# Kernel optimization log

Hardware: AMD Instinct MI355X
Metric: run time of the kernel (lower is better)

## Reference

```python
import jax, jax.numpy as jnp
import numpy as np

BIN_SIZE = 256
TOP_K = 16


def setup_inputs() -> dict:
    key = jax.random.key(0)
    kx, kc = jax.random.split(key)
    x = jax.random.normal(kx, (2, 4096, 512), dtype=jnp.float32)
    codebook = jax.random.normal(kc, (512, 16), dtype=jnp.float32)  # (feature_dim, max_num_bins//2)
    return {"x": x, "codebook": codebook}


def reference(x, codebook):
    B, N, F = x.shape
    n_bins = N // BIN_SIZE  # 16
    # LSH bucket assignment: project onto random hyperplanes, pick argmax of [p, -p]
    mul = x @ codebook[:, : n_bins // 2]                      # (B, N, n_bins//2)
    cmul = jnp.concatenate([mul, -mul], axis=-1)              # (B, N, n_bins)
    bin_idx = jnp.argmax(cmul, axis=-1)                       # (B, N)
    # argsort-based binning: equal-size bins of points sorted by bucket id
    bins_split = jnp.argsort(bin_idx, axis=-1).reshape(B, n_bins, BIN_SIZE)
    # gather points into bins: (B, n_bins, bin_size, F)
    points_binned = jnp.take_along_axis(x[:, None, :, :], bins_split[..., None], axis=2)
    # intra-bin dense similarity + sigmoid
    dm = jax.nn.sigmoid(jnp.einsum('bnif,bnjf->bnij', points_binned, points_binned))
    vals, idx = jax.lax.top_k(dm, TOP_K)                      # (B, n_bins, bin_size, k)
    # map local bin indices back to global point indices
    dst = jnp.take_along_axis(bins_split[:, :, None, :], idx, axis=-1)  # (B, nb, bs, k)
    src = jnp.broadcast_to(bins_split[..., None], dst.shape)
    b = jnp.broadcast_to(jnp.arange(B)[:, None, None, None], dst.shape)
    # dense equivalent of the coalesced batched sparse_coo_tensor of size (N, N)
    out = jnp.zeros((B, N, N), dtype=x.dtype).at[b, src, dst].add(vals)
    return out
```

## Files before the change

### kernel.cpp

```cpp
#include <hip/hip_runtime.h>
#include <stdint.h>
#include <math.h>

#define NPTS 4096
#define NF 512
#define NBINS 16
#define BSZ 256
#define TOPK 16
#define NBATCH 2
#define KSPLIT 4
#define SPART (NBATCH * NBINS * BSZ * BSZ)

typedef float vf4 __attribute__((ext_vector_type(4)));

__global__ __launch_bounds__(256) void k_assign(const float* __restrict__ x,
                                                const float* __restrict__ cb,
                                                int* __restrict__ bin_idx) {
    int gw   = (blockIdx.x * 256 + threadIdx.x) >> 6;
    int lane = threadIdx.x & 63;
    const float* row = x + (size_t)gw * NF;
    float acc[8];
#pragma unroll
    for (int j = 0; j < 8; j++) acc[j] = 0.f;
    for (int f = lane; f < NF; f += 64) {
        float xv = row[f];
        const float4* c = (const float4*)(cb + f * 16);
        float4 c0 = c[0], c1 = c[1];
        acc[0] += xv * c0.x; acc[1] += xv * c0.y; acc[2] += xv * c0.z; acc[3] += xv * c0.w;
        acc[4] += xv * c1.x; acc[5] += xv * c1.y; acc[6] += xv * c1.z; acc[7] += xv * c1.w;
    }
#pragma unroll
    for (int off = 32; off > 0; off >>= 1) {
#pragma unroll
        for (int j = 0; j < 8; j++) acc[j] += __shfl_xor(acc[j], off, 64);
    }
    if (lane == 0) {
        float best = acc[0]; int bi = 0;
#pragma unroll
        for (int j = 1; j < 8; j++) { if (acc[j] > best) { best = acc[j]; bi = j; } }
#pragma unroll
        for (int j = 0; j < 8; j++) { float v = -acc[j]; if (v > best) { best = v; bi = 8 + j; } }
        bin_idx[gw] = bi;
    }
}

__global__ __launch_bounds__(256) void k_sort(const int* __restrict__ bin_idx,
                                              int* __restrict__ order) {
    __shared__ int hist[NBINS][256];
    __shared__ int segsum[NBINS][16];
    __shared__ int segoff[NBINS][16];
    __shared__ int totals[NBINS];
    __shared__ int keybase[NBINS];
    int b = blockIdx.x, t = threadIdx.x;
    const int* bi = bin_idx + b * NPTS;
#pragma unroll
    for (int j = 0; j < NBINS; j++) hist[j][t] = 0;
    int base = t * 16;
    for (int i = 0; i < 16; i++) { int k = bi[base + i]; hist[k][t]++; }
    __syncthreads();
    {
        int j = t >> 4, sg = t & 15, s = 0;
#pragma unroll
        for (int u = 0; u < 16; u++) s += hist[j][sg * 16 + u];
        segsum[j][sg] = s;
    }
    __syncthreads();
    if (t < NBINS) {
        int run = 0;
#pragma unroll
        for (int sg = 0; sg < 16; sg++) { int c = segsum[t][sg]; segoff[t][sg] = run; run += c; }
        totals[t] = run;
    }
    __syncthreads();
    if (t == 0) {
        int run = 0;
#pragma unroll
        for (int j = 0; j < NBINS; j++) { keybase[j] = run; run += totals[j]; }
    }
    __syncthreads();
    {
        int j = t >> 4, sg = t & 15;
        int run = segoff[j][sg];
#pragma unroll
        for (int u = 0; u < 16; u++) { int c = hist[j][sg * 16 + u]; hist[j][sg * 16 + u] = run; run += c; }
    }
    __syncthreads();
    int* ob = order + b * NPTS;
    for (int i = 0; i < 16; i++) {
        int k = bi[base + i];
        int o = hist[k][t];
        hist[k][t] = o + 1;
        ob[keybase[k] + o] = base + i;
    }
}

__global__ __launch_bounds__(256, 2) void k_gemm(const float* __restrict__ x,
                                                 const int* __restrict__ order,
                                                 float* __restrict__ S) {
    int blk = blockIdx.x;
    int kh  = blk & 3;
    int tn  = (blk >> 2) & 1;
    int tm  = (blk >> 3) & 1;
    int bin = (blk >> 4) & 15;
    int b   = blk >> 8;
    int t  = threadIdx.x;
    int tx = t & 15, ty = t >> 4;
    __shared__ int   idxA[128];
    __shared__ int   idxB[128];
    __shared__ float Asl[32][132];
    __shared__ float Bsl[32][132];
    int ob = b * NPTS + bin * BSZ;
    if (t < 128) idxA[t] = order[ob + tm * 128 + t];
    else         idxB[t - 128] = order[ob + tn * 128 + (t - 128)];
    __syncthreads();
    const float* xb = x + (size_t)b * (NPTS * NF);
    int rowi = t & 127;
    int qb   = t >> 7;
    const float* rowA = xb + (size_t)idxA[rowi] * NF + kh * 128;
    const float* rowB = xb + (size_t)idxB[rowi] * NF + kh * 128;
    float acc[8][8];
#pragma unroll
    for (int i = 0; i < 8; i++)
#pragma unroll
        for (int j = 0; j < 8; j++) acc[i][j] = 0.f;
    float4 pa[4], pb[4];
#pragma unroll
    for (int l = 0; l < 4; l++) {
        pa[l] = *(const float4*)(rowA + (qb + 2 * l) * 4);
        pb[l] = *(const float4*)(rowB + (qb + 2 * l) * 4);
    }
    for (int it = 0; it < 4; it++) {
        __syncthreads();
#pragma unroll
        for (int l = 0; l < 4; l++) {
            int kq = (qb + 2 * l) * 4;
            Asl[kq + 0][rowi] = pa[l].x; Asl[kq + 1][rowi] = pa[l].y;
            Asl[kq + 2][rowi] = pa[l].z; Asl[kq + 3][rowi] = pa[l].w;
            Bsl[kq + 0][rowi] = pb[l].x; Bsl[kq + 1][rowi] = pb[l].y;
            Bsl[kq + 2][rowi] = pb[l].z; Bsl[kq + 3][rowi] = pb[l].w;
        }
        __syncthreads();
        if (it < 3) {
            const float* a2 = rowA + (it + 1) * 32;
            const float* b2 = rowB + (it + 1) * 32;
#pragma unroll
            for (int l = 0; l < 4; l++) {
                pa[l] = *(const float4*)(a2 + (qb + 2 * l) * 4);
                pb[l] = *(const float4*)(b2 + (qb + 2 * l) * 4);
            }
        }
#pragma unroll
        for (int kk = 0; kk < 32; kk++) {
            float4 a0 = *(const float4*)&Asl[kk][ty * 8];
            float4 a1 = *(const float4*)&Asl[kk][ty * 8 + 4];
            float4 b0 = *(const float4*)&Bsl[kk][tx * 8];
            float4 b1 = *(const float4*)&Bsl[kk][tx * 8 + 4];
            float av[8] = {a0.x, a0.y, a0.z, a0.w, a1.x, a1.y, a1.z, a1.w};
            float bv[8] = {b0.x, b0.y, b0.z, b0.w, b1.x, b1.y, b1.z, b1.w};
#pragma unroll
            for (int i = 0; i < 8; i++)
#pragma unroll
                for (int j = 0; j < 8; j++) acc[i][j] += av[i] * bv[j];
        }
    }
    float* Sp = S + (size_t)kh * SPART;
    size_t rowbase = (size_t)(b * NBINS + bin) * BSZ;
#pragma unroll
    for (int i = 0; i < 8; i++) {
        int r = tm * 128 + ty * 8 + i;
        float* orow = Sp + (rowbase + r) * BSZ + tn * 128 + tx * 8;
        *(float4*)(orow)     = make_float4(acc[i][0], acc[i][1], acc[i][2], acc[i][3]);
        *(float4*)(orow + 4) = make_float4(acc[i][4], acc[i][5], acc[i][6], acc[i][7]);
    }
}

__global__ __launch_bounds__(256) void k_topk(const float* __restrict__ S,
                                              const int* __restrict__ order,
                                              int* __restrict__ cols,
                                              float* __restrict__ vals) {
    int row  = (blockIdx.x * 256 + threadIdx.x) >> 6;
    int lane = threadIdx.x & 63;
    const float* s0 = S + (size_t)row * BSZ;
    unsigned long long key[4];
#pragma unroll
    for (int q = 0; q < 4; q++) {
        int j = lane + 64 * q;
        float d = s0[j] + s0[j + SPART] + s0[j + 2 * SPART] + s0[j + 3 * SPART];
        float v = 1.0f / (1.0f + expf(-d));
        key[q] = ((unsigned long long)__float_as_uint(v) << 32) | (unsigned)(255 - j);
    }
    int myj = 0; float myv = 0.f;
#pragma unroll
    for (int it = 0; it < TOPK; it++) {
        unsigned long long k = key[0];
        if (key[1] > k) k = key[1];
        if (key[2] > k) k = key[2];
        if (key[3] > k) k = key[3];
#pragma unroll
        for (int off = 32; off > 0; off >>= 1) {
            unsigned long long o = __shfl_xor(k, off, 64);
            if (o > k) k = o;
        }
        int jw = 255 - (int)(k & 0xFFull);
        if (lane == it) { myj = jw; myv = __uint_as_float((unsigned)(k >> 32)); }
        if ((jw & 63) == lane) {
            int q = jw >> 6;
            if      (q == 0) key[0] = 0ull;
            else if (q == 1) key[1] = 0ull;
            else if (q == 2) key[2] = 0ull;
            else             key[3] = 0ull;
        }
    }
    if (lane < TOPK) {
        int b   = row >> 12;
        int bin = (row >> 8) & 15;
        int i   = row & 255;
        const int* obp = order + b * NPTS + bin * BSZ;
        int srcg = obp[i];
        int dstg = obp[myj];
        int o = (b * NPTS + srcg) * TOPK + lane;
        cols[o] = dstg;
        vals[o] = myv;
    }
}

__global__ __launch_bounds__(256) void k_write(const int* __restrict__ cols,
                                               const float* __restrict__ vals,
                                               float* __restrict__ out) {
    __shared__ float buf[NPTS];
    __shared__ int   pc[TOPK];
    __shared__ float pv[TOPK];
    int row = blockIdx.x;
    int t   = threadIdx.x;
    if (t < TOPK) { pc[t] = cols[row * TOPK + t]; pv[t] = vals[row * TOPK + t]; }
    vf4 z = {0.f, 0.f, 0.f, 0.f};
#pragma unroll
    for (int u = 0; u < 4; u++) ((vf4*)buf)[u * 256 + t] = z;
    __syncthreads();
    if (t < TOPK) buf[pc[t]] = pv[t];
    __syncthreads();
    vf4* orow = (vf4*)(out + (size_t)row * NPTS);
#pragma unroll
    for (int u = 0; u < 4; u++) {
        __builtin_nontemporal_store(((const vf4*)buf)[u * 256 + t], &orow[u * 256 + t]);
    }
}

extern "C" void kernel_launch(void* const* d_in, const int* in_sizes, int n_in,
                              void* d_out, int out_size, void* d_ws, size_t ws_size,
                              hipStream_t stream) {
    const float* x  = (const float*)d_in[0];
    const float* cb = (const float*)d_in[1];
    float* out = (float*)d_out;
    int*   bin_idx = (int*)d_ws;
    int*   order   = bin_idx + NBATCH * NPTS;
    int*   cols    = order + NBATCH * NPTS;
    float* vals    = (float*)(cols + NBATCH * NPTS * TOPK);
    float* S = out;

    k_assign<<<2048, 256, 0, stream>>>(x, cb, bin_idx);
    k_sort  <<<NBATCH, 256, 0, stream>>>(bin_idx, order);
    k_gemm  <<<512, 256, 0, stream>>>(x, order, S);
    k_topk  <<<2048, 256, 0, stream>>>(S, order, cols, vals);
    k_write <<<NBATCH * NPTS, 256, 0, stream>>>(cols, vals, out);
}
```

Baseline: 220.5 us.

## Fuse top-k selection with dense row write, move partial scores to workspace

Merges the top-k kernel and the dense output-row writer into one kernel with one 64-thread block per row. Each block selects its 16 winners, scatters them into a shared-memory row buffer and streams the 4096-wide row straight to the output. This removes the cols/vals round trip and one launch. The split-K score partials move from the output buffer to workspace so the fused kernel can write output while reading scores, which needs a larger workspace. The 64-thread blocks use a large shared buffer, which may limit occupancy.

```diff
diff --git a/kernel.cpp b/kernel.cpp
--- a/kernel.cpp
+++ b/kernel.cpp
@@ -8,7 +8,6 @@
 #define BSZ 256
 #define TOPK 16
 #define NBATCH 2
-#define KSPLIT 4
 #define SPART (NBATCH * NBINS * BSZ * BSZ)
 
 typedef float vf4 __attribute__((ext_vector_type(4)));
@@ -174,12 +173,12 @@
     }
 }
 
-__global__ __launch_bounds__(256) void k_topk(const float* __restrict__ S,
+__global__ __launch_bounds__(64) void k_topkw(const float* __restrict__ S,
                                               const int* __restrict__ order,
-                                              int* __restrict__ cols,
-                                              float* __restrict__ vals) {
-    int row  = (blockIdx.x * 256 + threadIdx.x) >> 6;
-    int lane = threadIdx.x & 63;
+                                              float* __restrict__ out) {
+    __shared__ float buf[NPTS];
+    int row  = blockIdx.x;
+    int lane = threadIdx.x;
     const float* s0 = S + (size_t)row * BSZ;
     unsigned long long key[4];
 #pragma unroll
@@ -189,7 +188,8 @@
         float v = 1.0f / (1.0f + expf(-d));
         key[q] = ((unsigned long long)__float_as_uint(v) << 32) | (unsigned)(255 - j);
     }
-    int myj = 0; float myv = 0.f;
+    int   wj[TOPK];
+    float wv[TOPK];
 #pragma unroll
     for (int it = 0; it < TOPK; it++) {
         unsigned long long k = key[0];
@@ -202,7 +202,8 @@
             if (o > k) k = o;
         }
         int jw = 255 - (int)(k & 0xFFull);
-        if (lane == it) { myj = jw; myv = __uint_as_float((unsigned)(k >> 32)); }
+        wj[it] = jw;
+        wv[it] = __uint_as_float((unsigned)(k >> 32));
         if ((jw & 63) == lane) {
             int q = jw >> 6;
             if      (q == 0) key[0] = 0ull;
@@ -211,38 +212,24 @@
             else             key[3] = 0ull;
         }
     }
-    if (lane < TOPK) {
-        int b   = row >> 12;
-        int bin = (row >> 8) & 15;
-        int i   = row & 255;
-        const int* obp = order + b * NPTS + bin * BSZ;
-        int srcg = obp[i];
-        int dstg = obp[myj];
-        int o = (b * NPTS + srcg) * TOPK + lane;
-        cols[o] = dstg;
-        vals[o] = myv;
-    }
-}
-
-__global__ __launch_bounds__(256) void k_write(const int* __restrict__ cols,
-                                               const float* __restrict__ vals,
-                                               float* __restrict__ out) {
-    __shared__ float buf[NPTS];
-    __shared__ int   pc[TOPK];
-    __shared__ float pv[TOPK];
-    int row = blockIdx.x;
-    int t   = threadIdx.x;
-    if (t < TOPK) { pc[t] = cols[row * TOPK + t]; pv[t] = vals[row * TOPK + t]; }
     vf4 z = {0.f, 0.f, 0.f, 0.f};
 #pragma unroll
-    for (int u = 0; u < 4; u++) ((vf4*)buf)[u * 256 + t] = z;
-    __syncthreads();
-    if (t < TOPK) buf[pc[t]] = pv[t];
-    __syncthreads();
-    vf4* orow = (vf4*)(out + (size_t)row * NPTS);
-#pragma unroll
-    for (int u = 0; u < 4; u++) {
-        __builtin_nontemporal_store(((const vf4*)buf)[u * 256 + t], &orow[u * 256 + t]);
+    for (int u = 0; u < 16; u++) ((vf4*)buf)[u * 64 + lane] = z;
+    int b   = row >> 12;
+    int bin = (row >> 8) & 15;
+    int i   = row & 255;
+    const int* obp = order + b * NPTS + bin * BSZ;
+    int srcg = obp[i];
+    __syncthreads();
+#pragma unroll
+    for (int it = 0; it < TOPK; it++) {
+        if (lane == it) buf[obp[wj[it]]] = wv[it];
+    }
+    __syncthreads();
+    vf4* orow = (vf4*)(out + ((size_t)b * NPTS + srcg) * NPTS);
+#pragma unroll
+    for (int u = 0; u < 16; u++) {
+        __builtin_nontemporal_store(((const vf4*)buf)[u * 64 + lane], &orow[u * 64 + lane]);
     }
 }
 
@@ -254,13 +241,10 @@
     float* out = (float*)d_out;
     int*   bin_idx = (int*)d_ws;
     int*   order   = bin_idx + NBATCH * NPTS;
-    int*   cols    = order + NBATCH * NPTS;
-    float* vals    = (float*)(cols + NBATCH * NPTS * TOPK);
-    float* S = out;
+    float* S       = (float*)d_ws + 4 * NBATCH * NPTS;
 
     k_assign<<<2048, 256, 0, stream>>>(x, cb, bin_idx);
     k_sort  <<<NBATCH, 256, 0, stream>>>(bin_idx, order);
     k_gemm  <<<512, 256, 0, stream>>>(x, order, S);
-    k_topk  <<<2048, 256, 0, stream>>>(S, order, cols, vals);
-    k_write <<<NBATCH * NPTS, 256, 0, stream>>>(cols, vals, out);
-}
+    k_topkw <<<NBATCH * NPTS * NBINS / 16, 64, 0, stream>>>(S, order, out);
+}
```

After: 208.9 us (median of 2 runs). 5.3% less time.
